# Kernel tuning notes

Measured on AMD Instinct MI355X. Metric: run time of the kernel, lower is better.

## Reference

```python
import jax, jax.numpy as jnp
import numpy as np

SCALE = 0.125          # feature stride 8
OUT = 7                # roi_align output size
SR = 2                 # sampling_ratio
BBW = (10.0, 10.0, 5.0, 5.0)   # torchvision BoxCoder weights
CLAMP = float(np.log(1000.0 / 16.0))
IMG_H, IMG_W = 800.0, 1088.0


def _bilinear(img, ys, xs):
    # img [C,H,W]; ys,xs [P] -> [C,P]
    C, H, W = img.shape
    y = jnp.clip(ys, 0.0, H - 1.0)
    x = jnp.clip(xs, 0.0, W - 1.0)
    y0 = jnp.floor(y); x0 = jnp.floor(x)
    y0i = y0.astype(jnp.int32); x0i = x0.astype(jnp.int32)
    y1i = jnp.minimum(y0i + 1, H - 1); x1i = jnp.minimum(x0i + 1, W - 1)
    ly = y - y0; lx = x - x0
    flat = img.reshape(C, H * W)
    g = lambda yi, xi: flat[:, yi * W + xi]
    return (g(y0i, x0i) * (1 - ly) * (1 - lx) + g(y0i, x1i) * (1 - ly) * lx
            + g(y1i, x0i) * ly * (1 - lx) + g(y1i, x1i) * ly * lx)


def _roi_align(features, boxes, roi_batch):
    # features [B,C,H,W], boxes [N,4] (image coords), roi_batch [N] -> [N,C,7,7]
    B, C, H, W = features.shape
    P = OUT * SR

    def one(b, box):
        x1, y1, x2, y2 = box[0] * SCALE, box[1] * SCALE, box[2] * SCALE, box[3] * SCALE
        rw = jnp.maximum(x2 - x1, 1.0)
        rh = jnp.maximum(y2 - y1, 1.0)
        bw = rw / OUT; bh = rh / OUT
        off = (jnp.arange(OUT)[:, None] + (jnp.arange(SR)[None, :] + 0.5) / SR).reshape(-1)  # [P]
        ys = y1 + off * bh
        xs = x1 + off * bw
        yy = jnp.repeat(ys, P)   # [P*P], y-major
        xx = jnp.tile(xs, P)
        v = _bilinear(features[b], yy, xx)                   # [C, P*P]
        return v.reshape(C, OUT, SR, OUT, SR).mean(axis=(2, 4))  # avg over samples

    return jax.vmap(one)(roi_batch, boxes)


def _decode(deltas, boxes):
    # deltas [N,K,4], boxes [N,4] -> [N,K,4]
    pw = boxes[:, 2] - boxes[:, 0]
    ph = boxes[:, 3] - boxes[:, 1]
    cx = boxes[:, 0] + 0.5 * pw
    cy = boxes[:, 1] + 0.5 * ph
    dx = deltas[..., 0] / BBW[0]; dy = deltas[..., 1] / BBW[1]
    dw = jnp.minimum(deltas[..., 2] / BBW[2], CLAMP)
    dh = jnp.minimum(deltas[..., 3] / BBW[3], CLAMP)
    pcx = dx * pw[:, None] + cx[:, None]
    pcy = dy * ph[:, None] + cy[:, None]
    pww = jnp.exp(dw) * pw[:, None]
    phh = jnp.exp(dh) * ph[:, None]
    out = jnp.stack([
        jnp.clip(pcx - 0.5 * pww, 0.0, IMG_W),
        jnp.clip(pcy - 0.5 * phh, 0.0, IMG_H),
        jnp.clip(pcx + 0.5 * pww, 0.0, IMG_W),
        jnp.clip(pcy + 0.5 * phh, 0.0, IMG_H),
    ], axis=-1)
    return out


def setup_inputs() -> dict:
    key = jax.random.key(0)
    ks = jax.random.split(key, 12)
    B, C, H, W, N, NC = 2, 256, 100, 136, 1000, 2
    features = jax.random.normal(ks[0], (B, C, H, W), jnp.float32)
    # valid proposal boxes in image coords
    cx = jax.random.uniform(ks[1], (N,)) * IMG_W
    cy = jax.random.uniform(ks[2], (N,)) * IMG_H
    bw = jax.random.uniform(ks[3], (N,)) * 240.0 + 16.0
    bh = jax.random.uniform(ks[4], (N,)) * 240.0 + 16.0
    x1 = jnp.clip(cx - 0.5 * bw, 0.0, IMG_W - 2.0)
    y1 = jnp.clip(cy - 0.5 * bh, 0.0, IMG_H - 2.0)
    x2 = jnp.clip(x1 + bw, x1 + 1.0, IMG_W - 1.0)
    y2 = jnp.clip(y1 + bh, y1 + 1.0, IMG_H - 1.0)
    boxes = jnp.stack([x1, y1, x2, y2], axis=-1).astype(jnp.float32)
    roi_batch = jax.random.randint(ks[5], (N,), 0, B, dtype=jnp.int32)
    D = C * OUT * OUT  # 12544
    HID = 1024
    s = 0.02
    fc1_w = jax.random.normal(ks[6], (D, HID), jnp.float32) * s
    fc1_b = jnp.zeros((HID,), jnp.float32)
    fc2_w = jax.random.normal(ks[7], (HID, HID), jnp.float32) * s
    fc2_b = jnp.zeros((HID,), jnp.float32)
    cls_w = jax.random.normal(ks[8], (HID, NC), jnp.float32) * s
    cls_b = jnp.zeros((NC,), jnp.float32)
    bbox_w = jax.random.normal(ks[9], (HID, NC * 4), jnp.float32) * s
    bbox_b = jnp.zeros((NC * 4,), jnp.float32)
    return {"features": features, "boxes": boxes, "roi_batch": roi_batch,
            "fc1_w": fc1_w, "fc1_b": fc1_b, "fc2_w": fc2_w, "fc2_b": fc2_b,
            "cls_w": cls_w, "cls_b": cls_b, "bbox_w": bbox_w, "bbox_b": bbox_b}


def reference(features, boxes, roi_batch, fc1_w, fc1_b, fc2_w, fc2_b, cls_w, cls_b, bbox_w, bbox_b):
    N = boxes.shape[0]
    feats = _roi_align(features, boxes, roi_batch).reshape(N, -1)  # [N, 12544]
    h = jax.nn.relu(feats @ fc1_w + fc1_b)                         # TwoMLPHead fc6
    h = jax.nn.relu(h @ fc2_w + fc2_b)                             # TwoMLPHead fc7
    scores = jax.nn.softmax(h @ cls_w + cls_b, axis=-1)            # [N, 2]
    deltas = (h @ bbox_w + bbox_b).reshape(N, -1, 4)               # [N, 2, 4]
    dec = _decode(deltas, boxes).reshape(N, -1)                    # [N, 8]
    return jnp.concatenate([dec, scores], axis=-1)                 # [N, 10]
```

## Files before the change

### kernel.cpp

```cpp
#include <hip/hip_runtime.h>
#include <hip/hip_bf16.h>

#define BF16 __hip_bfloat16

typedef __bf16 bf16x8 __attribute__((ext_vector_type(8)));
typedef float floatx4 __attribute__((ext_vector_type(4)));

typedef const __attribute__((address_space(1))) void GV;
typedef __attribute__((address_space(3))) void LV;
#define GLD16(gp, lp) __builtin_amdgcn_global_load_lds((GV*)(gp), (LV*)(lp), 16, 0, 0)

__global__ __launch_bounds__(256) void t_feat(const float* __restrict__ features,
                                              BF16* __restrict__ featT) {
    __shared__ float tile[64][33];
    int bid = blockIdx.x;
    int z = bid / 1700, r = bid - z * 1700;
    int cx = r % 425, cy = r / 425;
    const int R = 256, C = 13600;
    const float* ip = features + (size_t)z * 256 * 13600;
    BF16* op = featT + (size_t)z * 256 * 13600;

    int tx = threadIdx.x & 31, ty = threadIdx.x >> 5;
    int r0 = cy << 6, c0 = cx << 5;
#pragma unroll
    for (int i = 0; i < 8; ++i)
        tile[ty + i * 8][tx] = ip[(size_t)(r0 + ty + i * 8) * C + c0 + tx];
    __syncthreads();
#pragma unroll
    for (int i = 0; i < 4; ++i) {
        int c = ty + i * 8;
        BF16 a = __float2bfloat16(tile[tx * 2][c]);
        BF16 b = __float2bfloat16(tile[tx * 2 + 1][c]);
        unsigned int pk = (unsigned int)*(unsigned short*)&a |
                          ((unsigned int)*(unsigned short*)&b << 16);
        *(unsigned int*)(op + (size_t)(c0 + c) * R + r0 + tx * 2) = pk;
    }
}

__global__ __launch_bounds__(256) void roi_and_wt(const BF16* __restrict__ featT,
                                                  const float* __restrict__ boxes,
                                                  const int* __restrict__ roi_batch,
                                                  BF16* __restrict__ feats,
                                                  const float* __restrict__ fc1_w,
                                                  const float* __restrict__ fc2_w,
                                                  BF16* __restrict__ w1t,
                                                  BF16* __restrict__ w2t) {
    __shared__ __align__(16) char smem[31360];
    int bid = blockIdx.x;
    int t = threadIdx.x;

    if (bid >= 1024) {
        float (*tile)[33] = (float(*)[33])smem;
        int r = bid - 1024;
        const float* ip;
        BF16* op;
        int R, C, cx, cy;
        if (r < 6272) {
            cx = r & 31; cy = r >> 5;
            R = 12544; C = 1024;
            ip = fc1_w; op = w1t;
        } else {
            r -= 6272;
            cx = r & 31; cy = r >> 5;
            R = 1024; C = 1024;
            ip = fc2_w; op = w2t;
        }
        int tx = t & 31, ty = t >> 5;
        int r0 = cy << 6, c0 = cx << 5;
#pragma unroll
        for (int i = 0; i < 8; ++i)
            tile[ty + i * 8][tx] = ip[(size_t)(r0 + ty + i * 8) * C + c0 + tx];
        __syncthreads();
#pragma unroll
        for (int i = 0; i < 4; ++i) {
            int c = ty + i * 8;
            BF16 a = __float2bfloat16(tile[tx * 2][c]);
            BF16 b = __float2bfloat16(tile[tx * 2 + 1][c]);
            unsigned int pk = (unsigned int)*(unsigned short*)&a |
                              ((unsigned int)*(unsigned short*)&b << 16);
            *(unsigned int*)(op + (size_t)(c0 + c) * R + r0 + tx * 2) = pk;
        }
        return;
    }

    int   (*s_off)[4] = (int(*)[4])smem;
    float (*s_w)[4]   = (float(*)[4])(smem + 3136);
    BF16* lbuf        = (BF16*)(smem + 6272);

    int roi = bid;
    BF16* orow = feats + (size_t)roi * 12544;
    if (roi >= 1000) {
        uint4* o4 = (uint4*)orow;
        uint4 z = {0u, 0u, 0u, 0u};
        for (int i = t; i < 1568; i += 256) o4[i] = z;
        return;
    }
    int b = roi_batch[roi];

    if (t < 196) {
        float x1 = boxes[roi * 4 + 0] * 0.125f;
        float y1 = boxes[roi * 4 + 1] * 0.125f;
        float x2 = boxes[roi * 4 + 2] * 0.125f;
        float y2 = boxes[roi * 4 + 3] * 0.125f;
        float bw = fmaxf(x2 - x1, 1.0f) * (1.0f / 7.0f);
        float bh = fmaxf(y2 - y1, 1.0f) * (1.0f / 7.0f);
        int cell = t >> 2, s = t & 3;
        int oy = cell / 7, ox = cell - oy * 7;
        int sy = s >> 1, sx = s & 1;
        float yc = y1 + ((float)oy + ((float)sy + 0.5f) * 0.5f) * bh;
        float xc = x1 + ((float)ox + ((float)sx + 0.5f) * 0.5f) * bw;
        yc = fminf(fmaxf(yc, 0.0f), 99.0f);
        xc = fminf(fmaxf(xc, 0.0f), 135.0f);
        float y0f = floorf(yc), x0f = floorf(xc);
        int y0 = (int)y0f, x0 = (int)x0f;
        int y1i = min(y0 + 1, 99), x1i = min(x0 + 1, 135);
        float ly = yc - y0f, lx = xc - x0f;
        s_w[t][0] = (1.0f - ly) * (1.0f - lx) * 0.25f;
        s_w[t][1] = (1.0f - ly) * lx * 0.25f;
        s_w[t][2] = ly * (1.0f - lx) * 0.25f;
        s_w[t][3] = ly * lx * 0.25f;
        s_off[t][0] = (y0 * 136 + x0) * 256;
        s_off[t][1] = (y0 * 136 + x1i) * 256;
        s_off[t][2] = (y1i * 136 + x0) * 256;
        s_off[t][3] = (y1i * 136 + x1i) * 256;
    }
    __syncthreads();

    int cb = t & 31, g = t >> 5;
    const BF16* fb = featT + (size_t)b * (100 * 136 * 256) + cb * 8;
    int chbase = cb * 8;
    for (int cell = g; cell < 49; cell += 8) {
        float a[8];
#pragma unroll
        for (int j = 0; j < 8; ++j) a[j] = 0.0f;
#pragma unroll
        for (int s = 0; s < 4; ++s) {
            int p = cell * 4 + s;
#pragma unroll
            for (int tap = 0; tap < 4; ++tap) {
                float w = s_w[p][tap];
                bf16x8 v = *(const bf16x8*)(fb + s_off[p][tap]);
#pragma unroll
                for (int j = 0; j < 8; ++j) a[j] += w * (float)v[j];
            }
        }
#pragma unroll
        for (int j = 0; j < 8; ++j)
            lbuf[(chbase + j) * 49 + cell] = __float2bfloat16(a[j]);
    }
    __syncthreads();
    uint4* o4 = (uint4*)orow;
    const uint4* l4 = (const uint4*)lbuf;
    for (int i = t; i < 1568; i += 256) o4[i] = l4[i];
}

#define STAGE_TILE(kbi, bj)                                                     \
    do {                                                                        \
        size_t ko_ = (size_t)(kbi) * 128;                                       \
        _Pragma("unroll")                                                       \
        for (int i_ = 0; i_ < 4; ++i_) {                                        \
            GLD16(gA + (size_t)(i_ * 8) * strideA + ko_,                        \
                  &lds[bj][0][lw + i_ * 1024]);                                 \
            GLD16(gB + (size_t)(i_ * 8) * strideA + ko_,                        \
                  &lds[bj][1][lw + i_ * 1024]);                                 \
        }                                                                       \
    } while (0)

__global__ __launch_bounds__(256) void gemm_splitk(const BF16* __restrict__ A,
                                                   const BF16* __restrict__ Bt,
                                                   float* __restrict__ P,
                                                   int K, int chunk) {
    __shared__ char lds[2][2][16384];
    int b = blockIdx.x;
    int L = (b & 7) * (gridDim.x >> 3) + (b >> 3);
    int tn = L & 7, tm = (L >> 3) & 7, s = L >> 6;

    int w = threadIdx.x >> 6, l = threadIdx.x & 63;
    int wm = w & 1, wn = w >> 1;
    int k0 = s * chunk;

    floatx4 acc[4][4];
#pragma unroll
    for (int i = 0; i < 4; ++i)
#pragma unroll
        for (int j = 0; j < 4; ++j) acc[i][j] = (floatx4){0.f, 0.f, 0.f, 0.f};

    const size_t strideA = (size_t)K * 2;
    int r8 = l >> 3;
    int g8 = (l & 7) ^ r8;
    const char* gA = (const char*)A + (size_t)(tm * 128 + w * 32 + r8) * strideA
                     + (size_t)k0 * 2 + (size_t)g8 * 16;
    const char* gB = (const char*)Bt + (size_t)(tn * 128 + w * 32 + r8) * strideA
                     + (size_t)k0 * 2 + (size_t)g8 * 16;
    int lw = w * 4096 + l * 16;

    int c = l & 15, q = l >> 4;
    int xa0 = ((0 * 4 + q) ^ (c & 7)) * 16;
    int xa1 = ((1 * 4 + q) ^ (c & 7)) * 16;
    int abase = (wm * 64 + c) * 128;
    int bbase = (wn * 64 + c) * 128;

    int nIter = chunk >> 6;

    STAGE_TILE(0, 0);

    for (int kb = 0; kb < nIter; ++kb) {
        int cur = kb & 1;
        if (kb + 1 < nIter) {
            STAGE_TILE(kb + 1, cur ^ 1);
            asm volatile("s_waitcnt vmcnt(8)" ::: "memory");
        } else {
            asm volatile("s_waitcnt vmcnt(0)" ::: "memory");
        }
        __builtin_amdgcn_sched_barrier(0);
        __builtin_amdgcn_s_barrier();
        __builtin_amdgcn_sched_barrier(0);

        const char* bufA = lds[cur][0];
        const char* bufB = lds[cur][1];
#pragma unroll
        for (int kk = 0; kk < 2; ++kk) {
            int xo = kk ? xa1 : xa0;
            bf16x8 af[4], bfr[4];
#pragma unroll
            for (int mi = 0; mi < 4; ++mi) af[mi] = *(const bf16x8*)(bufA + abase + mi * 2048 + xo);
#pragma unroll
            for (int ni = 0; ni < 4; ++ni) bfr[ni] = *(const bf16x8*)(bufB + bbase + ni * 2048 + xo);
#pragma unroll
            for (int mi = 0; mi < 4; ++mi)
#pragma unroll
                for (int ni = 0; ni < 4; ++ni)
                    acc[mi][ni] = __builtin_amdgcn_mfma_f32_16x16x32_bf16(af[mi], bfr[ni], acc[mi][ni], 0, 0, 0);
        }
        __builtin_amdgcn_sched_barrier(0);
        __builtin_amdgcn_s_barrier();
    }

    size_t base = (size_t)s << 20;
#pragma unroll
    for (int mi = 0; mi < 4; ++mi) {
        int rowG = tm * 128 + wm * 64 + mi * 16 + q * 4;
#pragma unroll
        for (int ni = 0; ni < 4; ++ni) {
            int colG = tn * 128 + wn * 64 + ni * 16 + c;
#pragma unroll
            for (int r = 0; r < 4; ++r)
                P[base + (size_t)(rowG + r) * 1024 + colG] = acc[mi][ni][r];
        }
    }
}

__global__ __launch_bounds__(256) void gemm_fc2(const BF16* __restrict__ A,
                                                const BF16* __restrict__ Bt,
                                                const float* __restrict__ bias,
                                                float* __restrict__ H) {
    __shared__ char lds[2][2][16384];
    int b = blockIdx.x;
    int L = (b & 7) * 8 + (b >> 3);
    int tn = L & 7, tm = L >> 3;

    int w = threadIdx.x >> 6, l = threadIdx.x & 63;
    int wm = w & 1, wn = w >> 1;

    floatx4 acc[4][4];
#pragma unroll
    for (int i = 0; i < 4; ++i)
#pragma unroll
        for (int j = 0; j < 4; ++j) acc[i][j] = (floatx4){0.f, 0.f, 0.f, 0.f};

    const size_t strideA = 2048;
    int r8 = l >> 3;
    int g8 = (l & 7) ^ r8;
    const char* gA = (const char*)A + (size_t)(tm * 128 + w * 32 + r8) * strideA
                     + (size_t)g8 * 16;
    const char* gB = (const char*)Bt + (size_t)(tn * 128 + w * 32 + r8) * strideA
                     + (size_t)g8 * 16;
    int lw = w * 4096 + l * 16;

    int c = l & 15, q = l >> 4;
    int xa0 = ((0 * 4 + q) ^ (c & 7)) * 16;
    int xa1 = ((1 * 4 + q) ^ (c & 7)) * 16;
    int abase = (wm * 64 + c) * 128;
    int bbase = (wn * 64 + c) * 128;

    const int nIter = 16;

    STAGE_TILE(0, 0);

    for (int kb = 0; kb < nIter; ++kb) {
        int cur = kb & 1;
        if (kb + 1 < nIter) {
            STAGE_TILE(kb + 1, cur ^ 1);
            asm volatile("s_waitcnt vmcnt(8)" ::: "memory");
        } else {
            asm volatile("s_waitcnt vmcnt(0)" ::: "memory");
        }
        __builtin_amdgcn_sched_barrier(0);
        __builtin_amdgcn_s_barrier();
        __builtin_amdgcn_sched_barrier(0);

        const char* bufA = lds[cur][0];
        const char* bufB = lds[cur][1];
#pragma unroll
        for (int kk = 0; kk < 2; ++kk) {
            int xo = kk ? xa1 : xa0;
            bf16x8 af[4], bfr[4];
#pragma unroll
            for (int mi = 0; mi < 4; ++mi) af[mi] = *(const bf16x8*)(bufA + abase + mi * 2048 + xo);
#pragma unroll
            for (int ni = 0; ni < 4; ++ni) bfr[ni] = *(const bf16x8*)(bufB + bbase + ni * 2048 + xo);
#pragma unroll
            for (int mi = 0; mi < 4; ++mi)
#pragma unroll
                for (int ni = 0; ni < 4; ++ni)
                    acc[mi][ni] = __builtin_amdgcn_mfma_f32_16x16x32_bf16(af[mi], bfr[ni], acc[mi][ni], 0, 0, 0);
        }
        __builtin_amdgcn_sched_barrier(0);
        __builtin_amdgcn_s_barrier();
    }

#pragma unroll
    for (int mi = 0; mi < 4; ++mi) {
        int rowG = tm * 128 + wm * 64 + mi * 16 + q * 4;
#pragma unroll
        for (int ni = 0; ni < 4; ++ni) {
            int colG = tn * 128 + wn * 64 + ni * 16 + c;
            float bv = bias[colG];
#pragma unroll
            for (int r = 0; r < 4; ++r)
                H[(size_t)(rowG + r) * 1024 + colG] = fmaxf(acc[mi][ni][r] + bv, 0.0f);
        }
    }
}

__global__ __launch_bounds__(256) void reduce_k(const float* __restrict__ P,
                                                const float* __restrict__ bias,
                                                BF16* __restrict__ out,
                                                int S) {
    int i = blockIdx.x * 256 + threadIdx.x;
    float a = bias[i & 1023];
    for (int s = 0; s < S; ++s) a += P[((size_t)s << 20) + i];
    a = fmaxf(a, 0.0f);
    out[i] = __float2bfloat16(a);
}

__global__ __launch_bounds__(256) void head_k(const float* __restrict__ H,
                                              const float* __restrict__ cls_w,
                                              const float* __restrict__ cls_b,
                                              const float* __restrict__ bbox_w,
                                              const float* __restrict__ bbox_b,
                                              const float* __restrict__ boxes,
                                              float* __restrict__ out) {
    __shared__ float red[4][10];
    int roi = blockIdx.x;
    int t = threadIdx.x, w = t >> 6, l = t & 63;
    int k4 = t * 4;

    floatx4 h = *(const floatx4*)(H + (size_t)roi * 1024 + k4);

    float acc[10];
#pragma unroll
    for (int j = 0; j < 10; ++j) acc[j] = 0.0f;
    floatx4 c0 = *(const floatx4*)(cls_w + k4 * 2);
    floatx4 c1 = *(const floatx4*)(cls_w + k4 * 2 + 4);
    acc[0] = h.x * c0.x + h.y * c0.z + h.z * c1.x + h.w * c1.z;
    acc[1] = h.x * c0.y + h.y * c0.w + h.z * c1.y + h.w * c1.w;
    const float* bw = bbox_w + k4 * 8;
#pragma unroll
    for (int kk = 0; kk < 4; ++kk) {
        float hv = (kk == 0) ? h.x : (kk == 1) ? h.y : (kk == 2) ? h.z : h.w;
        floatx4 b0 = *(const floatx4*)(bw + kk * 8);
        floatx4 b1 = *(const floatx4*)(bw + kk * 8 + 4);
        acc[2] += hv * b0.x; acc[3] += hv * b0.y; acc[4] += hv * b0.z; acc[5] += hv * b0.w;
        acc[6] += hv * b1.x; acc[7] += hv * b1.y; acc[8] += hv * b1.z; acc[9] += hv * b1.w;
    }
#pragma unroll
    for (int j = 0; j < 10; ++j) {
#pragma unroll
        for (int off = 32; off > 0; off >>= 1) acc[j] += __shfl_down(acc[j], off);
    }
    if (l == 0) {
#pragma unroll
        for (int j = 0; j < 10; ++j) red[w][j] = acc[j];
    }
    __syncthreads();
    if (t == 0) {
        float f[10];
#pragma unroll
        for (int j = 0; j < 10; ++j) f[j] = red[0][j] + red[1][j] + red[2][j] + red[3][j];
        float s0 = f[0] + cls_b[0], s1 = f[1] + cls_b[1];
        float m = fmaxf(s0, s1);
        float e0 = expf(s0 - m), e1 = expf(s1 - m);
        float inv = 1.0f / (e0 + e1);

        float bx1 = boxes[roi * 4 + 0], by1 = boxes[roi * 4 + 1];
        float bx2 = boxes[roi * 4 + 2], by2 = boxes[roi * 4 + 3];
        float pw = bx2 - bx1, ph = by2 - by1;
        float cx = bx1 + 0.5f * pw, cy = by1 + 0.5f * ph;
        const float CLAMPV = 4.135166556742356f;
        float* orow = out + roi * 10;
#pragma unroll
        for (int cl = 0; cl < 2; ++cl) {
            float dx = (f[2 + cl * 4 + 0] + bbox_b[cl * 4 + 0]) * 0.1f;
            float dy = (f[2 + cl * 4 + 1] + bbox_b[cl * 4 + 1]) * 0.1f;
            float dw = fminf((f[2 + cl * 4 + 2] + bbox_b[cl * 4 + 2]) * 0.2f, CLAMPV);
            float dh = fminf((f[2 + cl * 4 + 3] + bbox_b[cl * 4 + 3]) * 0.2f, CLAMPV);
            float pcx = dx * pw + cx, pcy = dy * ph + cy;
            float pww = expf(dw) * pw, phh = expf(dh) * ph;
            orow[cl * 4 + 0] = fminf(fmaxf(pcx - 0.5f * pww, 0.0f), 1088.0f);
            orow[cl * 4 + 1] = fminf(fmaxf(pcy - 0.5f * phh, 0.0f), 800.0f);
            orow[cl * 4 + 2] = fminf(fmaxf(pcx + 0.5f * pww, 0.0f), 1088.0f);
            orow[cl * 4 + 3] = fminf(fmaxf(pcy + 0.5f * phh, 0.0f), 800.0f);
        }
        orow[8] = e0 * inv;
        orow[9] = e1 * inv;
    }
}

extern "C" void kernel_launch(void* const* d_in, const int* in_sizes, int n_in,
                              void* d_out, int out_size, void* d_ws, size_t ws_size,
                              hipStream_t stream) {
    const float* features = (const float*)d_in[0];
    const float* boxes    = (const float*)d_in[1];
    const int*   roi_b    = (const int*)d_in[2];
    const float* fc1_w    = (const float*)d_in[3];
    const float* fc1_b    = (const float*)d_in[4];
    const float* fc2_w    = (const float*)d_in[5];
    const float* fc2_b    = (const float*)d_in[6];
    const float* cls_w    = (const float*)d_in[7];
    const float* cls_b    = (const float*)d_in[8];
    const float* bbox_w   = (const float*)d_in[9];
    const float* bbox_b   = (const float*)d_in[10];
    float* out = (float*)d_out;

    char* ws = (char*)d_ws;
    BF16* featT = (BF16*)(ws + 0);
    BF16* w1t   = (BF16*)(ws + 13926400);
    BF16* w2t   = (BF16*)(ws + 39616512);
    BF16* feats = (BF16*)(ws + 41713664);
    BF16* h1    = (BF16*)(ws + 67403776);
    float* P1   = (float*)(ws + 69500928);
    float* H2   = (float*)(ws + 0);

    int S1 = 7;

    t_feat<<<3400, 256, 0, stream>>>(features, featT);

    roi_and_wt<<<7808, 256, 0, stream>>>(featT, boxes, roi_b, feats,
                                         fc1_w, fc2_w, w1t, w2t);

    gemm_splitk<<<64 * S1, 256, 0, stream>>>(feats, w1t, P1, 12544, 12544 / S1);
    reduce_k<<<4096, 256, 0, stream>>>(P1, fc1_b, h1, S1);

    gemm_fc2<<<64, 256, 0, stream>>>(h1, w2t, fc2_b, H2);

    head_k<<<1000, 256, 0, stream>>>(H2, cls_w, cls_b, bbox_w, bbox_b, boxes, out);
}
```

Baseline: 207.5 us.

## Split-K the fc2 GEMM with atomics and interleave ROI and transpose blocks

The fc2 GEMM now splits K four ways, launching 256 blocks instead of 64, and accumulates partial results with float atomic adds into H2. reduce_k zeroes H2 beforehand, and head_k now applies the fc2 bias and ReLU. Separately, roi_and_wt interleaves ROI-align blocks among the weight-transpose blocks, one in every seven, so the heavier ROI work is spread across the grid instead of front-loaded. The split-K change fills more CUs but adds atomic traffic and a non-deterministic summation order.

```diff
diff --git a/kernel.cpp b/kernel.cpp
--- a/kernel.cpp
+++ b/kernel.cpp
@@ -49,9 +49,12 @@
     int bid = blockIdx.x;
     int t = threadIdx.x;
 
-    if (bid >= 1024) {
+    int bdiv7 = bid / 7;
+    bool is_roi = (bid < 7168) && (bid - bdiv7 * 7 == 0);
+
+    if (!is_roi) {
+        int r = (bid < 7168) ? (bid - bdiv7 - 1) : (6144 + bid - 7168);
         float (*tile)[33] = (float(*)[33])smem;
-        int r = bid - 1024;
         const float* ip;
         BF16* op;
         int R, C, cx, cy;
@@ -87,7 +90,7 @@
     float (*s_w)[4]   = (float(*)[4])(smem + 3136);
     BF16* lbuf        = (BF16*)(smem + 6272);
 
-    int roi = bid;
+    int roi = bdiv7;
     BF16* orow = feats + (size_t)roi * 12544;
     if (roi >= 1000) {
         uint4* o4 = (uint4*)orow;
@@ -252,15 +255,15 @@
 
 __global__ __launch_bounds__(256) void gemm_fc2(const BF16* __restrict__ A,
                                                 const BF16* __restrict__ Bt,
-                                                const float* __restrict__ bias,
                                                 float* __restrict__ H) {
     __shared__ char lds[2][2][16384];
     int b = blockIdx.x;
-    int L = (b & 7) * 8 + (b >> 3);
-    int tn = L & 7, tm = L >> 3;
+    int L = (b & 7) * 32 + (b >> 3);
+    int tn = L & 7, tm = (L >> 3) & 7, s = L >> 6;
 
     int w = threadIdx.x >> 6, l = threadIdx.x & 63;
     int wm = w & 1, wn = w >> 1;
+    int k0 = s * 256;
 
     floatx4 acc[4][4];
 #pragma unroll
@@ -272,9 +275,9 @@
     int r8 = l >> 3;
     int g8 = (l & 7) ^ r8;
     const char* gA = (const char*)A + (size_t)(tm * 128 + w * 32 + r8) * strideA
-                     + (size_t)g8 * 16;
+                     + (size_t)k0 * 2 + (size_t)g8 * 16;
     const char* gB = (const char*)Bt + (size_t)(tn * 128 + w * 32 + r8) * strideA
-                     + (size_t)g8 * 16;
+                     + (size_t)k0 * 2 + (size_t)g8 * 16;
     int lw = w * 4096 + l * 16;
 
     int c = l & 15, q = l >> 4;
@@ -283,7 +286,7 @@
     int abase = (wm * 64 + c) * 128;
     int bbase = (wn * 64 + c) * 128;
 
-    const int nIter = 16;
+    const int nIter = 4;
 
     STAGE_TILE(0, 0);
 
@@ -325,10 +328,9 @@
 #pragma unroll
         for (int ni = 0; ni < 4; ++ni) {
             int colG = tn * 128 + wn * 64 + ni * 16 + c;
-            float bv = bias[colG];
 #pragma unroll
             for (int r = 0; r < 4; ++r)
-                H[(size_t)(rowG + r) * 1024 + colG] = fmaxf(acc[mi][ni][r] + bv, 0.0f);
+                unsafeAtomicAdd(&H[(size_t)(rowG + r) * 1024 + colG], acc[mi][ni][r]);
         }
     }
 }
@@ -336,15 +338,18 @@
 __global__ __launch_bounds__(256) void reduce_k(const float* __restrict__ P,
                                                 const float* __restrict__ bias,
                                                 BF16* __restrict__ out,
+                                                float* __restrict__ H2z,
                                                 int S) {
     int i = blockIdx.x * 256 + threadIdx.x;
     float a = bias[i & 1023];
     for (int s = 0; s < S; ++s) a += P[((size_t)s << 20) + i];
     a = fmaxf(a, 0.0f);
     out[i] = __float2bfloat16(a);
+    H2z[i] = 0.0f;
 }
 
 __global__ __launch_bounds__(256) void head_k(const float* __restrict__ H,
+                                              const float* __restrict__ fc2_b,
                                               const float* __restrict__ cls_w,
                                               const float* __restrict__ cls_b,
                                               const float* __restrict__ bbox_w,
@@ -357,6 +362,9 @@
     int k4 = t * 4;
 
     floatx4 h = *(const floatx4*)(H + (size_t)roi * 1024 + k4);
+    floatx4 bb = *(const floatx4*)(fc2_b + k4);
+    h.x = fmaxf(h.x + bb.x, 0.f); h.y = fmaxf(h.y + bb.y, 0.f);
+    h.z = fmaxf(h.z + bb.z, 0.f); h.w = fmaxf(h.w + bb.w, 0.f);
 
     float acc[10];
 #pragma unroll
@@ -450,9 +458,9 @@
                                          fc1_w, fc2_w, w1t, w2t);
 
     gemm_splitk<<<64 * S1, 256, 0, stream>>>(feats, w1t, P1, 12544, 12544 / S1);
-    reduce_k<<<4096, 256, 0, stream>>>(P1, fc1_b, h1, S1);
-
-    gemm_fc2<<<64, 256, 0, stream>>>(h1, w2t, fc2_b, H2);
-
-    head_k<<<1000, 256, 0, stream>>>(H2, cls_w, cls_b, bbox_w, bbox_b, boxes, out);
-}
+    reduce_k<<<4096, 256, 0, stream>>>(P1, fc1_b, h1, H2, S1);
+
+    gemm_fc2<<<256, 256, 0, stream>>>(h1, w2t, H2);
+
+    head_k<<<1000, 256, 0, stream>>>(H2, fc2_b, cls_w, cls_b, bbox_w, bbox_b, boxes, out);
+}
```

Measured after the change: 219.3 us. +5.7%, slower.
